# Performance work log

Hardware: AMD Instinct MI355X
Metric: run time of the kernel (lower is better)

Reference implementation:

```python
import jax, jax.numpy as jnp
import numpy as np

V = 100000   # vocab_size
H = 128      # hidden_dim
B = 4096     # number of sentences in the batch
T = 409600


def setup_inputs() -> dict:
    key = jax.random.key(0)
    k_tok, k_seg, k_y, k_e, k_wh, k_bh, k_wo, k_bo = jax.random.split(key, 8)
    token_ids = jax.random.randint(k_tok, (T,), 0, V, dtype=jnp.int32)
    segment_ids = jnp.sort(jax.random.randint(k_seg, (T,), 0, B, dtype=jnp.int32))
    y_true = jax.random.uniform(k_y, (B,), dtype=jnp.float32)
    # learned parameters (nn.Embedding ~ N(0,1); Linear ~ U(-1/sqrt(fan_in), +))
    embed_table = jax.random.normal(k_e, (V, H), dtype=jnp.float32)
    lim = 1.0 / np.sqrt(H)
    W_hid = jax.random.uniform(k_wh, (H, H), minval=-lim, maxval=lim, dtype=jnp.float32)
    b_hid = jax.random.uniform(k_bh, (H,), minval=-lim, maxval=lim, dtype=jnp.float32)
    W_out = jax.random.uniform(k_wo, (H, 1), minval=-lim, maxval=lim, dtype=jnp.float32)
    b_out = jax.random.uniform(k_bo, (1,), minval=-lim, maxval=lim, dtype=jnp.float32)
    return {
        "token_ids": token_ids,
        "segment_ids": segment_ids,
        "y_true": y_true,
        "embed_table": embed_table,
        "W_hid": W_hid,
        "b_hid": b_hid,
        "W_out": W_out,
        "b_out": b_out,
    }


def reference(token_ids, segment_ids, y_true, embed_table, W_hid, b_hid, W_out, b_out):
    # Fused gather + segment-mean (replaces the per-sentence Python loop).
    tok_emb = embed_table[token_ids]                                    # [T, H]
    sums = jax.ops.segment_sum(tok_emb, segment_ids, num_segments=B)   # [B, H]
    counts = jax.ops.segment_sum(jnp.ones((T,), tok_emb.dtype), segment_ids,
                                 num_segments=B)                        # [B]
    sent_embeds = sums / jnp.maximum(counts, 1.0)[:, None]             # [B, H]
    # Small MLP head: tanh hidden -> sigmoid scalar score.
    hid = jnp.tanh(sent_embeds @ W_hid + b_hid)                        # [B, H]
    probas = jax.nn.sigmoid(hid @ W_out + b_out).squeeze(-1)           # [B]
    # BCE with size_average=False (sum reduction); torch clamps log at -100.
    log_p = jnp.clip(jnp.log(probas), -100.0)
    log_1mp = jnp.clip(jnp.log1p(-probas), -100.0)
    total_loss = -jnp.sum(y_true * log_p + (1.0 - y_true) * log_1mp)
    return total_loss
```

## Files before the change

### kernel.cpp

```cpp
#include <hip/hip_runtime.h>
#include <math.h>

#define HDIM 128

__global__ __launch_bounds__(256) void seg_bounds_kernel(
    const int* __restrict__ seg, int* __restrict__ starts,
    int Tval, int Bval, float* __restrict__ out) {
    int t = blockIdx.x * blockDim.x + threadIdx.x;
    if (t >= Tval) return;
    int b = seg[t];
    int a = (t == 0) ? -1 : seg[t - 1];
    for (int s = a + 1; s <= b; ++s) starts[s] = t;
    if (t == Tval - 1) {
        for (int s = b + 1; s <= Bval; ++s) starts[s] = Tval;
    }
    if (t == 0) out[0] = 0.0f;
}

__global__ __launch_bounds__(256) void gather_mean_kernel(
    const int* __restrict__ tok, const float* __restrict__ emb,
    const int* __restrict__ starts, float* __restrict__ sent, int Bval) {
    __shared__ float4 part[2][32];

    int wave = threadIdx.x >> 6;
    int lane = threadIdx.x & 63;
    int segslot = wave >> 1;
    int parity  = wave & 1;
    int s = blockIdx.x * 2 + segslot;
    if (s >= Bval) s = Bval - 1;

    int t0 = starts[s];
    int t1 = starts[s + 1];
    int cnt = t1 - t0;

    int half = lane >> 5;
    int col  = lane & 31;
    int q = parity * 2 + half;

    float4 acc = make_float4(0.f, 0.f, 0.f, 0.f);

    int i = t0 + q;
    if (i + 12 < t1) {
        int ta = tok[i], tb = tok[i + 4], tc = tok[i + 8], td = tok[i + 12];
        for (;;) {
            float4 fa = ((const float4*)(emb + (size_t)ta * HDIM))[col];
            float4 fb = ((const float4*)(emb + (size_t)tb * HDIM))[col];
            float4 fc = ((const float4*)(emb + (size_t)tc * HDIM))[col];
            float4 fd = ((const float4*)(emb + (size_t)td * HDIM))[col];
            int ni = i + 16;
            bool more = (ni + 12 < t1);
            if (more) {
                ta = tok[ni]; tb = tok[ni + 4]; tc = tok[ni + 8]; td = tok[ni + 12];
            }
            acc.x += fa.x + fb.x + fc.x + fd.x;
            acc.y += fa.y + fb.y + fc.y + fd.y;
            acc.z += fa.z + fb.z + fc.z + fd.z;
            acc.w += fa.w + fb.w + fc.w + fd.w;
            i = ni;
            if (!more) break;
        }
    }
    for (; i < t1; i += 4) {
        int tt = tok[i];
        float4 f = ((const float4*)(emb + (size_t)tt * HDIM))[col];
        acc.x += f.x; acc.y += f.y; acc.z += f.z; acc.w += f.w;
    }

    acc.x += __shfl_xor(acc.x, 32);
    acc.y += __shfl_xor(acc.y, 32);
    acc.z += __shfl_xor(acc.z, 32);
    acc.w += __shfl_xor(acc.w, 32);

    if (parity == 1 && half == 0) part[segslot][col] = acc;
    __syncthreads();
    if (parity == 0 && half == 0) {
        float4 o = part[segslot][col];
        acc.x += o.x; acc.y += o.y; acc.z += o.z; acc.w += o.w;
        float inv = 1.0f / (float)(cnt > 0 ? cnt : 1);
        acc.x *= inv; acc.y *= inv; acc.z *= inv; acc.w *= inv;
        ((float4*)(sent + (size_t)s * HDIM))[col] = acc;
    }
}

__global__ __launch_bounds__(256) void mlp_loss_kernel(
    const float* __restrict__ sent, const float* __restrict__ Wh,
    const float* __restrict__ bh, const float* __restrict__ Wo,
    const float* __restrict__ bo, const float* __restrict__ y,
    float* __restrict__ out, int Bval, int nblocks) {
    __shared__ float Wlds[HDIM * HDIM];
    __shared__ float slds[4][4 * HDIM];
    __shared__ float lred[4];

    for (int idx = threadIdx.x; idx < HDIM * HDIM / 4; idx += 256)
        ((float4*)Wlds)[idx] = ((const float4*)Wh)[idx];
    __syncthreads();

    int wave = threadIdx.x >> 6;
    int lane = threadIdx.x & 63;
    int j0 = lane * 2;

    float bh0 = bh[j0], bh1 = bh[j0 + 1];
    float wo0 = Wo[j0], wo1 = Wo[j0 + 1];
    float bov = bo[0];
    float lsum = 0.0f;

    const float2* W2 = (const float2*)Wlds;
    float* myld = &slds[wave][0];

    for (int base0 = blockIdx.x * 16; base0 < Bval; base0 += nblocks * 16) {
        int base = base0 + wave * 4;
        int rem = Bval - base;
        int nseg = rem < 4 ? (rem < 0 ? 0 : rem) : 4;

        for (int r = 0; r < nseg; ++r) {
            float2 v = ((const float2*)(sent + (size_t)(base + r) * HDIM))[lane];
            ((float2*)(myld + r * HDIM))[lane] = v;
        }

        float a00 = bh0, a01 = bh1, a10 = bh0, a11 = bh1;
        float a20 = bh0, a21 = bh1, a30 = bh0, a31 = bh1;
        for (int i = 0; i < HDIM; ++i) {
            float2 w = W2[i * (HDIM / 2) + lane];
            float s0 = myld[0 * HDIM + i];
            float s1 = myld[1 * HDIM + i];
            float s2 = myld[2 * HDIM + i];
            float s3 = myld[3 * HDIM + i];
            a00 = fmaf(s0, w.x, a00); a01 = fmaf(s0, w.y, a01);
            a10 = fmaf(s1, w.x, a10); a11 = fmaf(s1, w.y, a11);
            a20 = fmaf(s2, w.x, a20); a21 = fmaf(s2, w.y, a21);
            a30 = fmaf(s3, w.x, a30); a31 = fmaf(s3, w.y, a31);
        }

        float pr0 = tanhf(a00) * wo0 + tanhf(a01) * wo1;
        float pr1 = tanhf(a10) * wo0 + tanhf(a11) * wo1;
        float pr2 = tanhf(a20) * wo0 + tanhf(a21) * wo1;
        float pr3 = tanhf(a30) * wo0 + tanhf(a31) * wo1;
        for (int m = 1; m < 64; m <<= 1) {
            pr0 += __shfl_xor(pr0, m);
            pr1 += __shfl_xor(pr1, m);
            pr2 += __shfl_xor(pr2, m);
            pr3 += __shfl_xor(pr3, m);
        }

        if (lane == 0) {
            float prs[4] = {pr0, pr1, pr2, pr3};
            for (int r = 0; r < nseg; ++r) {
                float z = prs[r] + bov;
                float p = 1.0f / (1.0f + expf(-z));
                float lp  = fmaxf(logf(p),     -100.0f);
                float l1p = fmaxf(log1pf(-p),  -100.0f);
                float yv = y[base + r];
                lsum -= yv * lp + (1.0f - yv) * l1p;
            }
        }
    }

    if (lane == 0) lred[wave] = lsum;
    __syncthreads();
    if (threadIdx.x == 0) {
        float tot = lred[0] + lred[1] + lred[2] + lred[3];
        atomicAdd(out, tot);
    }
}

extern "C" void kernel_launch(void* const* d_in, const int* in_sizes, int n_in,
                              void* d_out, int out_size, void* d_ws, size_t ws_size,
                              hipStream_t stream) {
    const int*   tok = (const int*)d_in[0];
    const int*   seg = (const int*)d_in[1];
    const float* y   = (const float*)d_in[2];
    const float* emb = (const float*)d_in[3];
    const float* Wh  = (const float*)d_in[4];
    const float* bh  = (const float*)d_in[5];
    const float* Wo  = (const float*)d_in[6];
    const float* bo  = (const float*)d_in[7];

    int T_ = in_sizes[0];
    int B_ = in_sizes[2];

    float* out = (float*)d_out;

    int* starts = (int*)d_ws;
    size_t starts_bytes = ((size_t)(B_ + 1) * sizeof(int) + 255) & ~(size_t)255;
    float* sent = (float*)((char*)d_ws + starts_bytes);

    seg_bounds_kernel<<<(T_ + 255) / 256, 256, 0, stream>>>(seg, starts, T_, B_, out);
    gather_mean_kernel<<<(B_ + 1) / 2, 256, 0, stream>>>(tok, emb, starts, sent, B_);
    int nblocks = (B_ + 15) / 16;
    if (nblocks > 256) nblocks = 256;
    mlp_loss_kernel<<<nblocks, 256, 0, stream>>>(sent, Wh, bh, Wo, bo, y, out, B_, nblocks);
}
```

Measured before the change: 137.2 us.

## Fuse gather-mean with MLP head and loss into one kernel

Merges the gather/segment-mean kernel and the MLP+BCE kernel into a single kernel. Each block keeps its two sentence means in shared memory, computes the 128x128 hidden layer by reading W_hid directly from global (L2-cached), and atomically adds its two-sentence loss. This removes one launch and the round trip of the sentence-embedding buffer. In exchange, every block re-reads the full W_hid matrix and issues one atomic per block, 2048 atomics instead of at most 256.

```diff
diff --git a/kernel.cpp b/kernel.cpp
--- a/kernel.cpp
+++ b/kernel.cpp
@@ -17,20 +17,26 @@
     if (t == 0) out[0] = 0.0f;
 }
 
-__global__ __launch_bounds__(256) void gather_mean_kernel(
+__global__ __launch_bounds__(256) void fused_gather_mlp_kernel(
     const int* __restrict__ tok, const float* __restrict__ emb,
-    const int* __restrict__ starts, float* __restrict__ sent, int Bval) {
+    const int* __restrict__ starts, const float* __restrict__ Wh,
+    const float* __restrict__ bh, const float* __restrict__ Wo,
+    const float* __restrict__ bo, const float* __restrict__ y,
+    float* __restrict__ out, int Bval) {
     __shared__ float4 part[2][32];
+    __shared__ __align__(16) float s_lds[2][HDIM];
+    __shared__ float part2[4][2];
 
     int wave = threadIdx.x >> 6;
     int lane = threadIdx.x & 63;
     int segslot = wave >> 1;
     int parity  = wave & 1;
-    int s = blockIdx.x * 2 + segslot;
-    if (s >= Bval) s = Bval - 1;
+    int s0 = blockIdx.x * 2;
+    int s = s0 + segslot;
+    int sc = (s < Bval) ? s : (Bval - 1);
 
-    int t0 = starts[s];
-    int t1 = starts[s + 1];
+    int t0 = starts[sc];
+    int t1 = starts[sc + 1];
     int cnt = t1 - t0;
 
     int half = lane >> 5;
@@ -75,91 +81,49 @@
     __syncthreads();
     if (parity == 0 && half == 0) {
         float4 o = part[segslot][col];
-        acc.x += o.x; acc.y += o.y; acc.z += o.z; acc.w += o.w;
         float inv = 1.0f / (float)(cnt > 0 ? cnt : 1);
-        acc.x *= inv; acc.y *= inv; acc.z *= inv; acc.w *= inv;
-        ((float4*)(sent + (size_t)s * HDIM))[col] = acc;
+        float4 m;
+        m.x = (acc.x + o.x) * inv;
+        m.y = (acc.y + o.y) * inv;
+        m.z = (acc.z + o.z) * inv;
+        m.w = (acc.w + o.w) * inv;
+        ((float4*)s_lds[segslot])[col] = m;
     }
-}
-
-__global__ __launch_bounds__(256) void mlp_loss_kernel(
-    const float* __restrict__ sent, const float* __restrict__ Wh,
-    const float* __restrict__ bh, const float* __restrict__ Wo,
-    const float* __restrict__ bo, const float* __restrict__ y,
-    float* __restrict__ out, int Bval, int nblocks) {
-    __shared__ float Wlds[HDIM * HDIM];
-    __shared__ float slds[4][4 * HDIM];
-    __shared__ float lred[4];
-
-    for (int idx = threadIdx.x; idx < HDIM * HDIM / 4; idx += 256)
-        ((float4*)Wlds)[idx] = ((const float4*)Wh)[idx];
     __syncthreads();
 
-    int wave = threadIdx.x >> 6;
-    int lane = threadIdx.x & 63;
-    int j0 = lane * 2;
+    int mcol = wave * 32 + (lane & 31);
+    int mseg = lane >> 5;
+    const float* sv = s_lds[mseg];
 
-    float bh0 = bh[j0], bh1 = bh[j0 + 1];
-    float wo0 = Wo[j0], wo1 = Wo[j0 + 1];
-    float bov = bo[0];
-    float lsum = 0.0f;
+    float a = bh[mcol];
+    #pragma unroll 8
+    for (int k = 0; k < HDIM; ++k) {
+        a = fmaf(sv[k], Wh[k * HDIM + mcol], a);
+    }
+    float h = tanhf(a);
+    float pc = h * Wo[mcol];
+    pc += __shfl_xor(pc, 1);
+    pc += __shfl_xor(pc, 2);
+    pc += __shfl_xor(pc, 4);
+    pc += __shfl_xor(pc, 8);
+    pc += __shfl_xor(pc, 16);
+    if ((lane & 31) == 0) part2[wave][mseg] = pc;
+    __syncthreads();
 
-    const float2* W2 = (const float2*)Wlds;
-    float* myld = &slds[wave][0];
-
-    for (int base0 = blockIdx.x * 16; base0 < Bval; base0 += nblocks * 16) {
-        int base = base0 + wave * 4;
-        int rem = Bval - base;
-        int nseg = rem < 4 ? (rem < 0 ? 0 : rem) : 4;
-
-        for (int r = 0; r < nseg; ++r) {
-            float2 v = ((const float2*)(sent + (size_t)(base + r) * HDIM))[lane];
-            ((float2*)(myld + r * HDIM))[lane] = v;
-        }
-
-        float a00 = bh0, a01 = bh1, a10 = bh0, a11 = bh1;
-        float a20 = bh0, a21 = bh1, a30 = bh0, a31 = bh1;
-        for (int i = 0; i < HDIM; ++i) {
-            float2 w = W2[i * (HDIM / 2) + lane];
-            float s0 = myld[0 * HDIM + i];
-            float s1 = myld[1 * HDIM + i];
-            float s2 = myld[2 * HDIM + i];
-            float s3 = myld[3 * HDIM + i];
-            a00 = fmaf(s0, w.x, a00); a01 = fmaf(s0, w.y, a01);
-            a10 = fmaf(s1, w.x, a10); a11 = fmaf(s1, w.y, a11);
-            a20 = fmaf(s2, w.x, a20); a21 = fmaf(s2, w.y, a21);
-            a30 = fmaf(s3, w.x, a30); a31 = fmaf(s3, w.y, a31);
-        }
-
-        float pr0 = tanhf(a00) * wo0 + tanhf(a01) * wo1;
-        float pr1 = tanhf(a10) * wo0 + tanhf(a11) * wo1;
-        float pr2 = tanhf(a20) * wo0 + tanhf(a21) * wo1;
-        float pr3 = tanhf(a30) * wo0 + tanhf(a31) * wo1;
-        for (int m = 1; m < 64; m <<= 1) {
-            pr0 += __shfl_xor(pr0, m);
-            pr1 += __shfl_xor(pr1, m);
-            pr2 += __shfl_xor(pr2, m);
-            pr3 += __shfl_xor(pr3, m);
-        }
-
-        if (lane == 0) {
-            float prs[4] = {pr0, pr1, pr2, pr3};
-            for (int r = 0; r < nseg; ++r) {
-                float z = prs[r] + bov;
+    if (threadIdx.x == 0) {
+        float bov = bo[0];
+        float lsum = 0.0f;
+        for (int g = 0; g < 2; ++g) {
+            if (s0 + g < Bval) {
+                float z = part2[0][g] + part2[1][g] + part2[2][g] + part2[3][g] + bov;
                 float p = 1.0f / (1.0f + expf(-z));
-                float lp  = fmaxf(logf(p),     -100.0f);
-                float l1p = fmaxf(log1pf(-p),  -100.0f);
-                float yv = y[base + r];
+                float lp  = fmaxf(logf(p),    -100.0f);
+                float l1p = fmaxf(log1pf(-p), -100.0f);
+                float yv = y[s0 + g];
                 lsum -= yv * lp + (1.0f - yv) * l1p;
             }
         }
-    }
-
-    if (lane == 0) lred[wave] = lsum;
-    __syncthreads();
-    if (threadIdx.x == 0) {
-        float tot = lred[0] + lred[1] + lred[2] + lred[3];
-        atomicAdd(out, tot);
+        atomicAdd(out, lsum);
     }
 }
 
@@ -181,12 +145,8 @@
     float* out = (float*)d_out;
 
     int* starts = (int*)d_ws;
-    size_t starts_bytes = ((size_t)(B_ + 1) * sizeof(int) + 255) & ~(size_t)255;
-    float* sent = (float*)((char*)d_ws + starts_bytes);
 
     seg_bounds_kernel<<<(T_ + 255) / 256, 256, 0, stream>>>(seg, starts, T_, B_, out);
-    gather_mean_kernel<<<(B_ + 1) / 2, 256, 0, stream>>>(tok, emb, starts, sent, B_);
-    int nblocks = (B_ + 15) / 16;
-    if (nblocks > 256) nblocks = 256;
-    mlp_loss_kernel<<<nblocks, 256, 0, stream>>>(sent, Wh, bh, Wo, bo, y, out, B_, nblocks);
+    fused_gather_mlp_kernel<<<(B_ + 1) / 2, 256, 0, stream>>>(
+        tok, emb, starts, Wh, bh, Wo, bo, y, out, B_);
 }
```

After: 145.3 us. 1.06x slower.
